# Kernel optimization log

Hardware: AMD Instinct MI355X
Metric: run time of the kernel (lower is better)

The kernel has to match this reference:

```python
import jax, jax.numpy as jnp
import numpy as np

D_MODEL = 512
N_HEADS = 8
D_HEAD = D_MODEL // N_HEADS


def setup_inputs() -> dict:
    key = jax.random.key(0)
    ks = jax.random.split(key, 10)
    B, N = 4, 2048
    s = 1.0 / np.sqrt(D_MODEL)
    inp = {
        'x': jax.random.normal(ks[0], (B, N, D_MODEL), jnp.float32),
        'attn_bias': jax.random.normal(ks[1], (B, 1, N, N), jnp.float32),
        'wq': jax.random.normal(ks[2], (D_MODEL, D_MODEL), jnp.float32) * s,
        'bq': jnp.zeros((D_MODEL,), jnp.float32),
        'wk': jax.random.normal(ks[3], (D_MODEL, D_MODEL), jnp.float32) * s,
        'bk': jnp.zeros((D_MODEL,), jnp.float32),
        'wv': jax.random.normal(ks[4], (D_MODEL, D_MODEL), jnp.float32) * s,
        'bv': jnp.zeros((D_MODEL,), jnp.float32),
        'wo': jax.random.normal(ks[5], (D_MODEL, D_MODEL), jnp.float32) * s,
        'bo': jnp.zeros((D_MODEL,), jnp.float32),
    }
    return inp


def reference(x, attn_bias, wq, bq, wk, bk, wv, bv, wo, bo):
    B, N, D = x.shape
    h, dh = N_HEADS, D_HEAD
    # projections; weights stored as (in, out) so y = x @ w + b
    q = (x @ wq + bq).reshape(B, N, h, dh).transpose(0, 2, 1, 3)  # (B,h,N,dh)
    k = (x @ wk + bk).reshape(B, N, h, dh).transpose(0, 2, 1, 3)
    v = (x @ wv + bv).reshape(B, N, h, dh).transpose(0, 2, 1, 3)
    scores = jnp.einsum('bhnd,bhmd->bhnm', q, k) / jnp.sqrt(jnp.float32(dh))
    scores = scores + attn_bias  # broadcast over heads
    attn = jax.nn.softmax(scores, axis=-1)
    out = jnp.einsum('bhnm,bhmd->bhnd', attn, v)
    out = out.transpose(0, 2, 1, 3).reshape(B, N, D)
    return out @ wo + bo
```

## Files before the change

kernel.cpp:

```cpp
#include <hip/hip_runtime.h>
#include <hip/hip_bf16.h>

typedef __bf16 bf16x8 __attribute__((ext_vector_type(8)));
typedef float f32x4 __attribute__((ext_vector_type(4)));
typedef float f32x16 __attribute__((ext_vector_type(16)));
using u16 = unsigned short;
using u32 = unsigned int;

#define LDSS 72
#define TILE (64 * LDSS)

__device__ __forceinline__ u16 f2bf(float f) {
  union { float f; u32 u; } v; v.f = f;
  u32 r = v.u + 0x7fffu + ((v.u >> 16) & 1u);
  return (u16)(r >> 16);
}

__device__ __forceinline__ u32 cvt_pk_bf16(float lo, float hi) {
  u32 r;
  asm("v_cvt_pk_bf16_f32 %0, %1, %2" : "=v"(r) : "v"(lo), "v"(hi));
  return r;
}

__global__ void cast_x_kernel(const float* __restrict__ x, u16* __restrict__ xb) {
  int i = (blockIdx.x * 256 + threadIdx.x) * 8;
  float4 f0 = *(const float4*)&x[i];
  float4 f1 = *(const float4*)&x[i + 4];
  u16 u[8];
  u[0] = f2bf(f0.x); u[1] = f2bf(f0.y); u[2] = f2bf(f0.z); u[3] = f2bf(f0.w);
  u[4] = f2bf(f1.x); u[5] = f2bf(f1.y); u[6] = f2bf(f1.z); u[7] = f2bf(f1.w);
  *(uint4*)&xb[i] = *(uint4*)u;
}

__global__ void cast_wT_kernel(const float* __restrict__ w0, const float* __restrict__ w1,
                               const float* __restrict__ w2, const float* __restrict__ w3,
                               u16* __restrict__ t0, u16* __restrict__ t1,
                               u16* __restrict__ t2, u16* __restrict__ t3) {
  int i = blockIdx.x * 256 + threadIdx.x;
  int wi = i >> 18;
  int r = i & 262143;
  int row = r >> 9, col = r & 511;
  const float* w; u16* t;
  if (wi == 0)      { w = w0; t = t0; }
  else if (wi == 1) { w = w1; t = t1; }
  else if (wi == 2) { w = w2; t = t2; }
  else              { w = w3; t = t3; }
  t[col * 512 + row] = f2bf(w[r]);
}

__global__ __launch_bounds__(256) void proj_kernel(
    const u16* __restrict__ xb,
    const u16* __restrict__ wqT, const u16* __restrict__ wkT, const u16* __restrict__ wvT,
    const float* __restrict__ bq, const float* __restrict__ bk, const float* __restrict__ bv,
    u16* __restrict__ Q, u16* __restrict__ K, u16* __restrict__ Vt) {
  __shared__ u16 Alds[64 * LDSS];
  __shared__ u16 Blds[64 * LDSS];
  int which = blockIdx.z;
  const u16* wT; const float* bias; u16* out;
  if (which == 0)      { wT = wqT; bias = bq; out = Q; }
  else if (which == 1) { wT = wkT; bias = bk; out = K; }
  else                 { wT = wvT; bias = bv; out = Vt; }

  int m0 = blockIdx.y * 64;
  int n0 = blockIdx.x * 64;
  int tid = threadIdx.x;
  int lane = tid & 63, w = tid >> 6;
  int wm = w >> 1, wn = w & 1;
  int l15 = lane & 15, l4 = lane >> 4;

  int r0 = tid >> 3, c8 = (tid & 7) * 8;

  uint4 ar0 = *(const uint4*)&xb[(m0 + r0) * 512 + c8];
  uint4 ar1 = *(const uint4*)&xb[(m0 + r0 + 32) * 512 + c8];
  uint4 br0 = *(const uint4*)&wT[(n0 + r0) * 512 + c8];
  uint4 br1 = *(const uint4*)&wT[(n0 + r0 + 32) * 512 + c8];

  f32x4 acc[2][2] = {};
  for (int ks = 0; ks < 8; ks++) {
    __syncthreads();
    *(uint4*)&Alds[r0 * LDSS + c8]        = ar0;
    *(uint4*)&Alds[(r0 + 32) * LDSS + c8] = ar1;
    *(uint4*)&Blds[r0 * LDSS + c8]        = br0;
    *(uint4*)&Blds[(r0 + 32) * LDSS + c8] = br1;
    __syncthreads();
    if (ks < 7) {
      int k0 = (ks + 1) * 64;
      ar0 = *(const uint4*)&xb[(m0 + r0) * 512 + k0 + c8];
      ar1 = *(const uint4*)&xb[(m0 + r0 + 32) * 512 + k0 + c8];
      br0 = *(const uint4*)&wT[(n0 + r0) * 512 + k0 + c8];
      br1 = *(const uint4*)&wT[(n0 + r0 + 32) * 512 + k0 + c8];
    }
#pragma unroll
    for (int kk = 0; kk < 2; kk++) {
      bf16x8 a[2], b[2];
#pragma unroll
      for (int f = 0; f < 2; f++) {
        a[f] = *(const bf16x8*)&Alds[(wm * 32 + f * 16 + l15) * LDSS + kk * 32 + l4 * 8];
        b[f] = *(const bf16x8*)&Blds[(wn * 32 + f * 16 + l15) * LDSS + kk * 32 + l4 * 8];
      }
#pragma unroll
      for (int fm = 0; fm < 2; fm++)
#pragma unroll
        for (int fn = 0; fn < 2; fn++) {
          if (which == 2)
            acc[fm][fn] = __builtin_amdgcn_mfma_f32_16x16x32_bf16(b[fn], a[fm], acc[fm][fn], 0, 0, 0);
          else
            acc[fm][fn] = __builtin_amdgcn_mfma_f32_16x16x32_bf16(a[fm], b[fn], acc[fm][fn], 0, 0, 0);
        }
    }
  }
  int bidx = m0 >> 11;
  int head = n0 >> 6;
  if (which == 2) {
#pragma unroll
    for (int fm = 0; fm < 2; fm++)
#pragma unroll
      for (int fn = 0; fn < 2; fn++)
#pragma unroll
        for (int r = 0; r < 4; r++) {
          int drow = wn * 32 + fn * 16 + l4 * 4 + r;
          int col  = wm * 32 + fm * 16 + l15;
          float vv = acc[fm][fn][r] + bias[n0 + drow];
          out[((size_t)(bidx * 8 + head) * 64 + drow) * 2048 + (m0 & 2047) + col] = f2bf(vv);
        }
  } else {
#pragma unroll
    for (int fm = 0; fm < 2; fm++)
#pragma unroll
      for (int fn = 0; fn < 2; fn++)
#pragma unroll
        for (int r = 0; r < 4; r++) {
          int row = wm * 32 + fm * 16 + l4 * 4 + r;
          int col = wn * 32 + fn * 16 + l15;
          int nrow = (m0 & 2047) + row;
          float vv = acc[fm][fn][r] + bias[n0 + col];
          out[(((size_t)(bidx * 8 + head) * 2048) + nrow) * 64 + col] = f2bf(vv);
        }
  }
}

__global__ __launch_bounds__(512, 2) void attn_kernel(
    const u16* __restrict__ Q, const u16* __restrict__ K, const u16* __restrict__ Vt,
    const float* __restrict__ bias, u16* __restrict__ O) {
  __shared__ u16 smem[4 * TILE];

  int qt = blockIdx.x, h = blockIdx.y, b = blockIdx.z;
  int tid = threadIdx.x;
  int lane = tid & 63, w = tid >> 6;
  int g2 = w >> 2, ww = w & 3;
  int l31 = lane & 31, hi = lane >> 5;
  int qrow = qt * 128 + ww * 32 + l31;

  const u16* Qbh  = Q  + (size_t)(b * 8 + h) * 2048 * 64;
  const u16* Kbh  = K  + (size_t)(b * 8 + h) * 2048 * 64;
  const u16* Vtbh = Vt + (size_t)(b * 8 + h) * 64 * 2048;
  const float* biasq = bias + (size_t)b * 2048 * 2048 + (size_t)qrow * 2048;

  u16* Kl = smem + g2 * TILE;
  u16* Vl = smem + (2 + g2) * TILE;
  const int tbase = g2 * 16;

  bf16x8 qf[4];
#pragma unroll
  for (int dk = 0; dk < 4; dk++)
    qf[dk] = *(const bf16x8*)&Qbh[qrow * 64 + dk * 16 + hi * 8];

  f32x16 o[2] = {};
  float mrow = -1e30f, lrow = 0.f;

  int tid2 = tid & 255;
  int r0 = tid2 >> 3, c8 = (tid2 & 7) * 8;

  uint4 kr0 = *(const uint4*)&Kbh[(tbase * 64 + r0) * 64 + c8];
  uint4 kr1 = *(const uint4*)&Kbh[(tbase * 64 + r0 + 32) * 64 + c8];
  uint4 vr0 = *(const uint4*)&Vtbh[r0 * 2048 + tbase * 64 + c8];
  uint4 vr1 = *(const uint4*)&Vtbh[(r0 + 32) * 2048 + tbase * 64 + c8];
  float4 bb0[4];
#pragma unroll
  for (int g = 0; g < 4; g++)
    bb0[g] = *(const float4*)&biasq[tbase * 64 + 8 * g + 4 * hi];

  for (int t = 0; t < 16; t++) {
    __syncthreads();
    *(uint4*)&Kl[r0 * LDSS + c8]        = kr0;
    *(uint4*)&Kl[(r0 + 32) * LDSS + c8] = kr1;
    *(uint4*)&Vl[r0 * LDSS + c8]        = vr0;
    *(uint4*)&Vl[(r0 + 32) * LDSS + c8] = vr1;
    __syncthreads();

    int tile = tbase + t;
    bool pf = (t < 15);

    f32x16 s[2] = {};
    __builtin_amdgcn_s_setprio(1);
#pragma unroll
    for (int dk = 0; dk < 4; dk++) {
      bf16x8 a0 = *(const bf16x8*)&Kl[l31 * LDSS + dk * 16 + hi * 8];
      s[0] = __builtin_amdgcn_mfma_f32_32x32x16_bf16(a0, qf[dk], s[0], 0, 0, 0);
      bf16x8 a1 = *(const bf16x8*)&Kl[(32 + l31) * LDSS + dk * 16 + hi * 8];
      s[1] = __builtin_amdgcn_mfma_f32_32x32x16_bf16(a1, qf[dk], s[1], 0, 0, 0);
    }
    __builtin_amdgcn_s_setprio(0);

    float4 b1[4];
#pragma unroll
    for (int g = 0; g < 4; g++)
      b1[g] = *(const float4*)&biasq[tile * 64 + 32 + 8 * g + 4 * hi];

    float mx[8];
#pragma unroll
    for (int g = 0; g < 4; g++) {
      float4 bv4 = bb0[g];
      float v0 = s[0][g * 4 + 0] * 0.125f + bv4.x;
      float v1 = s[0][g * 4 + 1] * 0.125f + bv4.y;
      float v2 = s[0][g * 4 + 2] * 0.125f + bv4.z;
      float v3 = s[0][g * 4 + 3] * 0.125f + bv4.w;
      s[0][g * 4 + 0] = v0; s[0][g * 4 + 1] = v1;
      s[0][g * 4 + 2] = v2; s[0][g * 4 + 3] = v3;
      mx[g] = fmaxf(fmaxf(v0, v1), fmaxf(v2, v3));
    }
#pragma unroll
    for (int g = 0; g < 4; g++) {
      float4 bv4 = b1[g];
      float v0 = s[1][g * 4 + 0] * 0.125f + bv4.x;
      float v1 = s[1][g * 4 + 1] * 0.125f + bv4.y;
      float v2 = s[1][g * 4 + 2] * 0.125f + bv4.z;
      float v3 = s[1][g * 4 + 3] * 0.125f + bv4.w;
      s[1][g * 4 + 0] = v0; s[1][g * 4 + 1] = v1;
      s[1][g * 4 + 2] = v2; s[1][g * 4 + 3] = v3;
      mx[4 + g] = fmaxf(fmaxf(v0, v1), fmaxf(v2, v3));
    }
    mx[0] = fmaxf(mx[0], mx[4]); mx[1] = fmaxf(mx[1], mx[5]);
    mx[2] = fmaxf(mx[2], mx[6]); mx[3] = fmaxf(mx[3], mx[7]);
    float m = fmaxf(fmaxf(mx[0], mx[1]), fmaxf(mx[2], mx[3]));
    m = fmaxf(m, __shfl_xor(m, 32));

    if (!__all(m <= mrow + 8.0f)) {
      float mnew = fmaxf(mrow, m);
      float corr = __expf(mrow - mnew);
      mrow = mnew;
      lrow *= corr;
#pragma unroll
      for (int dt = 0; dt < 2; dt++)
#pragma unroll
        for (int i = 0; i < 16; i++) o[dt][i] *= corr;
    }

    u32 c[2][8];
    float sm[8];
#pragma unroll
    for (int kt = 0; kt < 2; kt++)
#pragma unroll
      for (int g = 0; g < 4; g++) {
        float p0 = __expf(s[kt][g * 4 + 0] - mrow);
        float p1 = __expf(s[kt][g * 4 + 1] - mrow);
        float p2 = __expf(s[kt][g * 4 + 2] - mrow);
        float p3 = __expf(s[kt][g * 4 + 3] - mrow);
        sm[kt * 4 + g] = (p0 + p1) + (p2 + p3);
        c[kt][2 * g]     = cvt_pk_bf16(p0, p1);
        c[kt][2 * g + 1] = cvt_pk_bf16(p2, p3);
      }
    sm[0] += sm[4]; sm[1] += sm[5]; sm[2] += sm[6]; sm[3] += sm[7];
    float sum = (sm[0] + sm[1]) + (sm[2] + sm[3]);
    sum += __shfl_xor(sum, 32);
    lrow += sum;

    if (pf) {
      int kb = (tile + 1) * 64;
      kr0 = *(const uint4*)&Kbh[(kb + r0) * 64 + c8];
      kr1 = *(const uint4*)&Kbh[(kb + r0 + 32) * 64 + c8];
      vr0 = *(const uint4*)&Vtbh[r0 * 2048 + kb + c8];
      vr1 = *(const uint4*)&Vtbh[(r0 + 32) * 2048 + kb + c8];
#pragma unroll
      for (int g = 0; g < 4; g++)
        bb0[g] = *(const float4*)&biasq[kb + 8 * g + 4 * hi];
    }

    __builtin_amdgcn_s_setprio(1);
#pragma unroll
    for (int kk = 0; kk < 4; kk++) {
      const int kt = kk >> 1, jA = 4 * (kk & 1);
      u32 d0 = (u32)__shfl_xor((int)c[kt][jA + 0], 32);
      u32 d1 = (u32)__shfl_xor((int)c[kt][jA + 1], 32);
      u32 d2 = (u32)__shfl_xor((int)c[kt][jA + 2], 32);
      u32 d3 = (u32)__shfl_xor((int)c[kt][jA + 3], 32);
      union { u32 u[4]; bf16x8 v; } pfg;
      pfg.u[0] = hi ? d2 : c[kt][jA + 0];
      pfg.u[1] = hi ? d3 : c[kt][jA + 1];
      pfg.u[2] = hi ? c[kt][jA + 2] : d0;
      pfg.u[3] = hi ? c[kt][jA + 3] : d1;
#pragma unroll
      for (int dt = 0; dt < 2; dt++) {
        bf16x8 va = *(const bf16x8*)&Vl[(dt * 32 + l31) * LDSS + kk * 16 + hi * 8];
        o[dt] = __builtin_amdgcn_mfma_f32_32x32x16_bf16(va, pfg.v, o[dt], 0, 0, 0);
      }
    }
    __builtin_amdgcn_s_setprio(0);
  }

  __syncthreads();
  float* olds = (float*)smem;
  float2* mllds = (float2*)(smem + (4 * 32 * 64) * 2);

  if (g2 == 1) {
    mllds[ww * 64 + lane] = make_float2(mrow, lrow);
#pragma unroll
    for (int dt = 0; dt < 2; dt++)
#pragma unroll
      for (int i = 0; i < 16; i++)
        olds[(ww * 32 + dt * 16 + i) * 64 + lane] = o[dt][i];
  }
  __syncthreads();
  if (g2 == 0) {
    float2 ml = mllds[ww * 64 + lane];
    float M = fmaxf(mrow, ml.x);
    float w0 = __expf(mrow - M), w1 = __expf(ml.x - M);
    float linv = 1.0f / (lrow * w0 + ml.y * w1);
    float cw0 = w0 * linv, cw1 = w1 * linv;
    size_t obase = (size_t)(b * 2048 + qrow) * 512 + h * 64;
#pragma unroll
    for (int dt = 0; dt < 2; dt++)
#pragma unroll
      for (int g = 0; g < 4; g++) {
        float v0 = o[dt][4 * g + 0] * cw0 + olds[(ww * 32 + dt * 16 + 4 * g + 0) * 64 + lane] * cw1;
        float v1 = o[dt][4 * g + 1] * cw0 + olds[(ww * 32 + dt * 16 + 4 * g + 1) * 64 + lane] * cw1;
        float v2 = o[dt][4 * g + 2] * cw0 + olds[(ww * 32 + dt * 16 + 4 * g + 2) * 64 + lane] * cw1;
        float v3 = o[dt][4 * g + 3] * cw0 + olds[(ww * 32 + dt * 16 + 4 * g + 3) * 64 + lane] * cw1;
        uint2 pr;
        pr.x = cvt_pk_bf16(v0, v1);
        pr.y = cvt_pk_bf16(v2, v3);
        *(uint2*)&O[obase + dt * 32 + 8 * g + 4 * hi] = pr;
      }
  }
}

__global__ __launch_bounds__(256) void outproj_kernel(
    const u16* __restrict__ Ob, const u16* __restrict__ woT,
    const float* __restrict__ bo, float* __restrict__ out) {
  __shared__ u16 Alds[64 * LDSS];
  __shared__ u16 Blds[64 * LDSS];
  int m0 = blockIdx.y * 64;
  int n0 = blockIdx.x * 64;
  int tid = threadIdx.x;
  int lane = tid & 63, w = tid >> 6;
  int wm = w >> 1, wn = w & 1;
  int l15 = lane & 15, l4 = lane >> 4;

  int r0 = tid >> 3, c8 = (tid & 7) * 8;
  uint4 ar0 = *(const uint4*)&Ob[(m0 + r0) * 512 + c8];
  uint4 ar1 = *(const uint4*)&Ob[(m0 + r0 + 32) * 512 + c8];
  uint4 br0 = *(const uint4*)&woT[(n0 + r0) * 512 + c8];
  uint4 br1 = *(const uint4*)&woT[(n0 + r0 + 32) * 512 + c8];

  f32x4 acc[2][2] = {};
  for (int ks = 0; ks < 8; ks++) {
    __syncthreads();
    *(uint4*)&Alds[r0 * LDSS + c8]        = ar0;
    *(uint4*)&Alds[(r0 + 32) * LDSS + c8] = ar1;
    *(uint4*)&Blds[r0 * LDSS + c8]        = br0;
    *(uint4*)&Blds[(r0 + 32) * LDSS + c8] = br1;
    __syncthreads();
    if (ks < 7) {
      int k0 = (ks + 1) * 64;
      ar0 = *(const uint4*)&Ob[(m0 + r0) * 512 + k0 + c8];
      ar1 = *(const uint4*)&Ob[(m0 + r0 + 32) * 512 + k0 + c8];
      br0 = *(const uint4*)&woT[(n0 + r0) * 512 + k0 + c8];
      br1 = *(const uint4*)&woT[(n0 + r0 + 32) * 512 + k0 + c8];
    }
#pragma unroll
    for (int kk = 0; kk < 2; kk++) {
      bf16x8 a[2], bfr[2];
#pragma unroll
      for (int f = 0; f < 2; f++) {
        a[f] = *(const bf16x8*)&Alds[(wm * 32 + f * 16 + l15) * LDSS + kk * 32 + l4 * 8];
        bfr[f] = *(const bf16x8*)&Blds[(wn * 32 + f * 16 + l15) * LDSS + kk * 32 + l4 * 8];
      }
#pragma unroll
      for (int fm = 0; fm < 2; fm++)
#pragma unroll
        for (int fn = 0; fn < 2; fn++)
          acc[fm][fn] = __builtin_amdgcn_mfma_f32_16x16x32_bf16(a[fm], bfr[fn], acc[fm][fn], 0, 0, 0);
    }
  }
#pragma unroll
  for (int fm = 0; fm < 2; fm++)
#pragma unroll
    for (int fn = 0; fn < 2; fn++)
#pragma unroll
      for (int r = 0; r < 4; r++) {
        int row = wm * 32 + fm * 16 + l4 * 4 + r;
        int col = wn * 32 + fn * 16 + l15;
        out[(size_t)(m0 + row) * 512 + n0 + col] = acc[fm][fn][r] + bo[n0 + col];
      }
}

extern "C" void kernel_launch(void* const* d_in, const int* in_sizes, int n_in,
                              void* d_out, int out_size, void* d_ws, size_t ws_size,
                              hipStream_t stream) {
  const float* x    = (const float*)d_in[0];
  const float* bias = (const float*)d_in[1];
  const float* wq   = (const float*)d_in[2];
  const float* bq   = (const float*)d_in[3];
  const float* wk   = (const float*)d_in[4];
  const float* bk   = (const float*)d_in[5];
  const float* wv   = (const float*)d_in[6];
  const float* bv   = (const float*)d_in[7];
  const float* wo   = (const float*)d_in[8];
  const float* bo   = (const float*)d_in[9];
  float* out = (float*)d_out;

  char* ws = (char*)d_ws;
  u16* xb  = (u16*)(ws + 0);
  u16* wqT = (u16*)(ws + 8388608);
  u16* wkT = (u16*)(ws + 8912896);
  u16* wvT = (u16*)(ws + 9437184);
  u16* woT = (u16*)(ws + 9961472);
  u16* Qb  = (u16*)(ws + 10485760);
  u16* Kb  = (u16*)(ws + 18874368);
  u16* VtB = (u16*)(ws + 27262976);
  u16* Ob  = (u16*)(ws + 35651584);

  hipLaunchKernelGGL(cast_x_kernel, dim3(2048), dim3(256), 0, stream, x, xb);
  hipLaunchKernelGGL(cast_wT_kernel, dim3(4096), dim3(256), 0, stream,
                     wq, wk, wv, wo, wqT, wkT, wvT, woT);
  hipLaunchKernelGGL(proj_kernel, dim3(8, 128, 3), dim3(256), 0, stream,
                     xb, wqT, wkT, wvT, bq, bk, bv, Qb, Kb, VtB);
  hipLaunchKernelGGL(attn_kernel, dim3(16, 8, 4), dim3(512), 0, stream,
                     Qb, Kb, VtB, bias, Ob);
  hipLaunchKernelGGL(outproj_kernel, dim3(8, 128), dim3(256), 0, stream,
                     Ob, woT, bo, out);
}
```

Before: 148.2 us.

## Tile weight transpose through LDS, prefetch full bias tile, use exp2 softmax

The weight cast-transpose kernel now stages 64x64 tiles in shared memory, so both its reads and its writes are coalesced instead of scattered per-element stores. In attention, both halves of the bias tile are prefetched a tile ahead rather than loading the second half synchronously inside the loop. The softmax exponentials use v_exp_f32 with a fused multiply by log2(e) in place of __expf. The changes target global-memory latency and ALU cost, at the price of extra registers for the larger bias prefetch.

```diff
diff --git a/kernel.cpp b/kernel.cpp
--- a/kernel.cpp
+++ b/kernel.cpp
@@ -9,6 +9,7 @@
 
 #define LDSS 72
 #define TILE (64 * LDSS)
+#define LOG2E 1.4426950408889634f
 
 __device__ __forceinline__ u16 f2bf(float f) {
   union { float f; u32 u; } v; v.f = f;
@@ -19,6 +20,12 @@
 __device__ __forceinline__ u32 cvt_pk_bf16(float lo, float hi) {
   u32 r;
   asm("v_cvt_pk_bf16_f32 %0, %1, %2" : "=v"(r) : "v"(lo), "v"(hi));
+  return r;
+}
+
+__device__ __forceinline__ float exp2_fast(float x) {
+  float r;
+  asm("v_exp_f32 %0, %1" : "=v"(r) : "v"(x));
   return r;
 }
 
@@ -32,20 +39,36 @@
   *(uint4*)&xb[i] = *(uint4*)u;
 }
 
-__global__ void cast_wT_kernel(const float* __restrict__ w0, const float* __restrict__ w1,
-                               const float* __restrict__ w2, const float* __restrict__ w3,
-                               u16* __restrict__ t0, u16* __restrict__ t1,
-                               u16* __restrict__ t2, u16* __restrict__ t3) {
-  int i = blockIdx.x * 256 + threadIdx.x;
-  int wi = i >> 18;
-  int r = i & 262143;
-  int row = r >> 9, col = r & 511;
+__global__ __launch_bounds__(256) void cast_wT_kernel(
+    const float* __restrict__ w0, const float* __restrict__ w1,
+    const float* __restrict__ w2, const float* __restrict__ w3,
+    u16* __restrict__ t0, u16* __restrict__ t1,
+    u16* __restrict__ t2, u16* __restrict__ t3) {
+  __shared__ u16 tl[64][72];
+  int wi = blockIdx.z;
   const float* w; u16* t;
   if (wi == 0)      { w = w0; t = t0; }
   else if (wi == 1) { w = w1; t = t1; }
   else if (wi == 2) { w = w2; t = t2; }
   else              { w = w3; t = t3; }
-  t[col * 512 + row] = f2bf(w[r]);
+  int r0 = blockIdx.x * 64, c0 = blockIdx.y * 64;
+  int tid = threadIdx.x;
+  int row = tid >> 2, q = tid & 3;
+#pragma unroll
+  for (int j = 0; j < 4; j++) {
+    float4 f = *(const float4*)&w[(r0 + row) * 512 + c0 + q * 16 + j * 4];
+    tl[row][q * 16 + j * 4 + 0] = f2bf(f.x);
+    tl[row][q * 16 + j * 4 + 1] = f2bf(f.y);
+    tl[row][q * 16 + j * 4 + 2] = f2bf(f.z);
+    tl[row][q * 16 + j * 4 + 3] = f2bf(f.w);
+  }
+  __syncthreads();
+  int crow = tid >> 2;
+  u16 tmp[16];
+#pragma unroll
+  for (int j = 0; j < 16; j++) tmp[j] = tl[q * 16 + j][crow];
+  *(uint4*)&t[(c0 + crow) * 512 + r0 + q * 16]     = *(uint4*)&tmp[0];
+  *(uint4*)&t[(c0 + crow) * 512 + r0 + q * 16 + 8] = *(uint4*)&tmp[8];
 }
 
 __global__ __launch_bounds__(256) void proj_kernel(
@@ -175,10 +198,12 @@
   uint4 kr1 = *(const uint4*)&Kbh[(tbase * 64 + r0 + 32) * 64 + c8];
   uint4 vr0 = *(const uint4*)&Vtbh[r0 * 2048 + tbase * 64 + c8];
   uint4 vr1 = *(const uint4*)&Vtbh[(r0 + 32) * 2048 + tbase * 64 + c8];
-  float4 bb0[4];
-#pragma unroll
-  for (int g = 0; g < 4; g++)
-    bb0[g] = *(const float4*)&biasq[tbase * 64 + 8 * g + 4 * hi];
+  float4 bb[8];
+#pragma unroll
+  for (int kt = 0; kt < 2; kt++)
+#pragma unroll
+    for (int g = 0; g < 4; g++)
+      bb[kt * 4 + g] = *(const float4*)&biasq[tbase * 64 + kt * 32 + 8 * g + 4 * hi];
 
   for (int t = 0; t < 16; t++) {
     __syncthreads();
@@ -202,34 +227,20 @@
     }
     __builtin_amdgcn_s_setprio(0);
 
-    float4 b1[4];
-#pragma unroll
-    for (int g = 0; g < 4; g++)
-      b1[g] = *(const float4*)&biasq[tile * 64 + 32 + 8 * g + 4 * hi];
-
     float mx[8];
 #pragma unroll
-    for (int g = 0; g < 4; g++) {
-      float4 bv4 = bb0[g];
-      float v0 = s[0][g * 4 + 0] * 0.125f + bv4.x;
-      float v1 = s[0][g * 4 + 1] * 0.125f + bv4.y;
-      float v2 = s[0][g * 4 + 2] * 0.125f + bv4.z;
-      float v3 = s[0][g * 4 + 3] * 0.125f + bv4.w;
-      s[0][g * 4 + 0] = v0; s[0][g * 4 + 1] = v1;
-      s[0][g * 4 + 2] = v2; s[0][g * 4 + 3] = v3;
-      mx[g] = fmaxf(fmaxf(v0, v1), fmaxf(v2, v3));
-    }
-#pragma unroll
-    for (int g = 0; g < 4; g++) {
-      float4 bv4 = b1[g];
-      float v0 = s[1][g * 4 + 0] * 0.125f + bv4.x;
-      float v1 = s[1][g * 4 + 1] * 0.125f + bv4.y;
-      float v2 = s[1][g * 4 + 2] * 0.125f + bv4.z;
-      float v3 = s[1][g * 4 + 3] * 0.125f + bv4.w;
-      s[1][g * 4 + 0] = v0; s[1][g * 4 + 1] = v1;
-      s[1][g * 4 + 2] = v2; s[1][g * 4 + 3] = v3;
-      mx[4 + g] = fmaxf(fmaxf(v0, v1), fmaxf(v2, v3));
-    }
+    for (int kt = 0; kt < 2; kt++)
+#pragma unroll
+      for (int g = 0; g < 4; g++) {
+        float4 bv4 = bb[kt * 4 + g];
+        float v0 = s[kt][g * 4 + 0] * 0.125f + bv4.x;
+        float v1 = s[kt][g * 4 + 1] * 0.125f + bv4.y;
+        float v2 = s[kt][g * 4 + 2] * 0.125f + bv4.z;
+        float v3 = s[kt][g * 4 + 3] * 0.125f + bv4.w;
+        s[kt][g * 4 + 0] = v0; s[kt][g * 4 + 1] = v1;
+        s[kt][g * 4 + 2] = v2; s[kt][g * 4 + 3] = v3;
+        mx[kt * 4 + g] = fmaxf(fmaxf(v0, v1), fmaxf(v2, v3));
+      }
     mx[0] = fmaxf(mx[0], mx[4]); mx[1] = fmaxf(mx[1], mx[5]);
     mx[2] = fmaxf(mx[2], mx[6]); mx[3] = fmaxf(mx[3], mx[7]);
     float m = fmaxf(fmaxf(mx[0], mx[1]), fmaxf(mx[2], mx[3]));
@@ -237,7 +248,7 @@
 
     if (!__all(m <= mrow + 8.0f)) {
       float mnew = fmaxf(mrow, m);
-      float corr = __expf(mrow - mnew);
+      float corr = exp2_fast((mrow - mnew) * LOG2E);
       mrow = mnew;
       lrow *= corr;
 #pragma unroll
@@ -246,16 +257,17 @@
         for (int i = 0; i < 16; i++) o[dt][i] *= corr;
     }
 
+    float m2 = mrow * LOG2E;
     u32 c[2][8];
     float sm[8];
 #pragma unroll
     for (int kt = 0; kt < 2; kt++)
 #pragma unroll
       for (int g = 0; g < 4; g++) {
-        float p0 = __expf(s[kt][g * 4 + 0] - mrow);
-        float p1 = __expf(s[kt][g * 4 + 1] - mrow);
-        float p2 = __expf(s[kt][g * 4 + 2] - mrow);
-        float p3 = __expf(s[kt][g * 4 + 3] - mrow);
+        float p0 = exp2_fast(__builtin_fmaf(s[kt][g * 4 + 0], LOG2E, -m2));
+        float p1 = exp2_fast(__builtin_fmaf(s[kt][g * 4 + 1], LOG2E, -m2));
+        float p2 = exp2_fast(__builtin_fmaf(s[kt][g * 4 + 2], LOG2E, -m2));
+        float p3 = exp2_fast(__builtin_fmaf(s[kt][g * 4 + 3], LOG2E, -m2));
         sm[kt * 4 + g] = (p0 + p1) + (p2 + p3);
         c[kt][2 * g]     = cvt_pk_bf16(p0, p1);
         c[kt][2 * g + 1] = cvt_pk_bf16(p2, p3);
@@ -272,8 +284,10 @@
       vr0 = *(const uint4*)&Vtbh[r0 * 2048 + kb + c8];
       vr1 = *(const uint4*)&Vtbh[(r0 + 32) * 2048 + kb + c8];
 #pragma unroll
-      for (int g = 0; g < 4; g++)
-        bb0[g] = *(const float4*)&biasq[kb + 8 * g + 4 * hi];
+      for (int kt = 0; kt < 2; kt++)
+#pragma unroll
+        for (int g = 0; g < 4; g++)
+          bb[kt * 4 + g] = *(const float4*)&biasq[kb + kt * 32 + 8 * g + 4 * hi];
     }
 
     __builtin_amdgcn_s_setprio(1);
@@ -314,7 +328,7 @@
   if (g2 == 0) {
     float2 ml = mllds[ww * 64 + lane];
     float M = fmaxf(mrow, ml.x);
-    float w0 = __expf(mrow - M), w1 = __expf(ml.x - M);
+    float w0 = exp2_fast((mrow - M) * LOG2E), w1 = exp2_fast((ml.x - M) * LOG2E);
     float linv = 1.0f / (lrow * w0 + ml.y * w1);
     float cw0 = w0 * linv, cw1 = w1 * linv;
     size_t obase = (size_t)(b * 2048 + qrow) * 512 + h * 64;
@@ -421,7 +435,7 @@
   u16* Ob  = (u16*)(ws + 35651584);
 
   hipLaunchKernelGGL(cast_x_kernel, dim3(2048), dim3(256), 0, stream, x, xb);
-  hipLaunchKernelGGL(cast_wT_kernel, dim3(4096), dim3(256), 0, stream,
+  hipLaunchKernelGGL(cast_wT_kernel, dim3(8, 8, 4), dim3(256), 0, stream,
                      wq, wk, wv, wo, wqT, wkT, wvT, woT);
   hipLaunchKernelGGL(proj_kernel, dim3(8, 128, 3), dim3(256), 0, stream,
                      xb, wqT, wkT, wvT, bq, bk, bv, Qb, Kb, VtB);
```

After: 152.9 us. +3.2%, slower.
